# Optimization experiments

Hardware: AMD Instinct MI355X
Metric: run time of the kernel (lower is better)

Reference implementation:

```python
import jax, jax.numpy as jnp
import numpy as np

B, S, D = 8, 2048, 64
NEG = -1e9


def setup_inputs() -> dict:
    key = jax.random.key(0)
    kq, kk, kv = jax.random.split(key, 3)
    return {
        "queries": jax.random.normal(kq, (B, S, D), dtype=jnp.float32),
        "keys": jax.random.normal(kk, (B, S, D), dtype=jnp.float32),
        "values": jax.random.normal(kv, (B, S, D), dtype=jnp.float32),
        "mask_q": jnp.ones((B, S), dtype=jnp.float32),
        "mask_k": jnp.ones((B, S), dtype=jnp.float32),
        "mask_v": jnp.ones((B, S), dtype=jnp.float32),
    }


def reference(queries, keys, values, mask_q, mask_k, mask_v):
    # scaled QK^T: [B, Sq, Sk]
    scaler = jnp.sqrt(jnp.asarray(queries.shape[-1], dtype=queries.dtype))
    scores = jnp.einsum("bqd,bkd->bqk", queries, keys) / scaler
    # additive padding mask from outer product of query/key masks
    padding_mask = mask_q[:, :, None] * mask_k[:, None, :]  # [B, Sq, Sk]
    scores = scores + (1.0 - padding_mask) * NEG
    attention_weights = jax.nn.softmax(scores, axis=-1)
    # mask values then weighted sum
    values = values * mask_v[:, :, None]
    output = jnp.einsum("bqk,bkd->bqd", attention_weights, values)
    return output
```

## Files before the change

kernel.cpp:

```cpp
#include <hip/hip_runtime.h>
#include <math.h>

#define BATCH 8
#define SEQ   2048
#define DIM   64
#define NEGC  (-1e9f)

typedef short short8 __attribute__((ext_vector_type(8)));
typedef float f32x4  __attribute__((ext_vector_type(4)));

#define MFMA(a, b, c) __builtin_amdgcn_mfma_f32_16x16x32_bf16((a), (b), (c), 0, 0, 0)

__device__ __forceinline__ ushort f2bf(float x) {
    uint u = __float_as_uint(x);
    uint r = (u + 0x7fffu + ((u >> 16) & 1u)) >> 16;
    return (ushort)r;
}
__device__ __forceinline__ float bf2f(ushort h) {
    return __uint_as_float(((uint)h) << 16);
}

__global__ __launch_bounds__(256)
void prep_kv(const float* __restrict__ K, const float* __restrict__ V,
             const float* __restrict__ MV, ushort* __restrict__ ws) {
    const int gid = blockIdx.x * 256 + threadIdx.x;
    const int isV = gid >> 17;
    const int id  = gid & 131071;
    const int b   = id >> 14;
    const int rt  = id & 16383;
    const int t   = rt >> 9;
    const int r   = rt & 511;
    ushort* base = ws + (size_t)(b * 32 + t) * 12288;

    if (!isV) {
        const int mtc = r >> 6, qd = (r >> 4) & 3, mm = r & 15;
        const int mt = mtc >> 1, c = mtc & 1;
        const int key = t * 64 + mt * 16 + mm;
        const int d0  = c * 32 + qd * 8;
        const float* src = K + ((size_t)b * SEQ + key) * DIM + d0;
        float4 x0 = *(const float4*)src;
        float4 x1 = *(const float4*)(src + 4);
        float xs[8] = {x0.x, x0.y, x0.z, x0.w, x1.x, x1.y, x1.z, x1.w};
        short8 hv, lv;
#pragma unroll
        for (int j = 0; j < 8; j++) {
            ushort h = f2bf(xs[j]);
            hv[j] = (short)h;
            lv[j] = (short)f2bf(xs[j] - bf2f(h));
        }
        *(short8*)(base + r * 8)        = hv;
        *(short8*)(base + 4096 + r * 8) = lv;
    } else {
        const int kg5 = r >> 8, dg = (r >> 6) & 3, kq = (r >> 4) & 3, dm = r & 15;
        const int d  = dg * 16 + dm;
        const int k0 = t * 64 + kg5 * 32 + kq * 8;
        short8 ov;
#pragma unroll
        for (int j = 0; j < 8; j++) {
            const int key = k0 + j;
            float v = V[((size_t)b * SEQ + key) * DIM + d] * MV[(size_t)b * SEQ + key];
            ov[j] = (short)f2bf(v);
        }
        *(short8*)(base + 8192 + r * 8) = ov;
    }
}

__global__ __launch_bounds__(256, 2)
void attn_main(const float* __restrict__ Q, const float* __restrict__ MQ,
               const float* __restrict__ MK, const ushort* __restrict__ ws,
               float* __restrict__ O) {
    __shared__ __align__(16) ushort Stage[12288];
    __shared__ __align__(16) ushort Pf[4][512];
    __shared__ __align__(16) float  Msc[2][1280];

    const ushort* KfH = Stage;
    const ushort* KfL = Stage + 4096;
    const ushort* Vf  = Stage + 8192;

    const int t    = threadIdx.x;
    const int w    = t >> 6;
    const int lane = t & 63;
    const int quad = lane >> 4;
    const int lq   = lane & 15;
    const int qg   = w & 1;
    const int half = w >> 1;

    const int b  = blockIdx.x >> 6;
    const int q0 = (blockIdx.x & 63) * 32;
    const int q  = q0 + qg * 16 + lq;

    const float*  MKb = MK + (size_t)b * SEQ;
    const ushort* wsb = ws + (size_t)b * 32 * 12288;

    short8 qh[2], ql[2];
    {
        const float* Qr = Q + ((size_t)b * SEQ + q) * DIM;
#pragma unroll
        for (int c = 0; c < 2; c++) {
            float4 x0 = *(const float4*)(Qr + c * 32 + quad * 8);
            float4 x1 = *(const float4*)(Qr + c * 32 + quad * 8 + 4);
            float xs[8] = {x0.x, x0.y, x0.z, x0.w, x1.x, x1.y, x1.z, x1.w};
#pragma unroll
            for (int j = 0; j < 8; j++) {
                float v   = xs[j] * 0.125f;
                ushort hi = f2bf(v);
                ql[c][j]  = (short)f2bf(v - bf2f(hi));
                qh[c][j]  = (short)hi;
            }
        }
    }
    const float mq   = MQ[(size_t)b * SEQ + q];
    const float apen = NEGC * mq;

    float m = -1e30f, l = 0.0f;
    f32x4 ot0 = {0,0,0,0}, ot1 = {0,0,0,0}, ot2 = {0,0,0,0}, ot3 = {0,0,0,0};

    ushort* Pw   = Pf[w];
    const int kb = half * 32;

#pragma unroll 1
    for (int tile = 0; tile < 32; tile++) {
        const ushort* src = wsb + (size_t)tile * 12288;
#pragma unroll
        for (int u = 0; u < 6; u++) {
            const int off = (w * 64 + u * 256) * 8;
            __builtin_amdgcn_global_load_lds(
                (const __attribute__((address_space(1))) void*)(src + off + lane * 8),
                (__attribute__((address_space(3))) void*)(Stage + off),
                16, 0, 0);
        }
        __syncthreads();

        f32x4 st0 = {0,0,0,0}, st1 = {0,0,0,0};
        const int mtg = half * 2;
#pragma unroll
        for (int c = 0; c < 2; c++) {
            short8 a0h = *(const short8*)&KfH[((mtg + 0) * 2 + c) * 512 + lane * 8];
            short8 a0l = *(const short8*)&KfL[((mtg + 0) * 2 + c) * 512 + lane * 8];
            short8 a1h = *(const short8*)&KfH[((mtg + 1) * 2 + c) * 512 + lane * 8];
            short8 a1l = *(const short8*)&KfL[((mtg + 1) * 2 + c) * 512 + lane * 8];
            st0 = MFMA(a0h, qh[c], st0);
            st0 = MFMA(a0h, ql[c], st0);
            st0 = MFMA(a0l, qh[c], st0);
            st1 = MFMA(a1h, qh[c], st1);
            st1 = MFMA(a1h, ql[c], st1);
            st1 = MFMA(a1l, qh[c], st1);
        }

        const float* mkp = MKb + tile * 64 + kb + quad * 4;
        float4 mk0 = *(const float4*)mkp;
        float4 mk1 = *(const float4*)(mkp + 16);
        float mks0[4] = {mk0.x, mk0.y, mk0.z, mk0.w};
        float mks1[4] = {mk1.x, mk1.y, mk1.z, mk1.w};
        float s0[4], s1[4];
#pragma unroll
        for (int r = 0; r < 4; r++) {
            s0[r] = st0[r] + (NEGC - apen * mks0[r]);
            s1[r] = st1[r] + (NEGC - apen * mks1[r]);
        }
        float cm = s0[0];
#pragma unroll
        for (int r = 1; r < 4; r++) cm = fmaxf(cm, s0[r]);
#pragma unroll
        for (int r = 0; r < 4; r++) cm = fmaxf(cm, s1[r]);
        cm = fmaxf(cm, __shfl_xor(cm, 16));
        cm = fmaxf(cm, __shfl_xor(cm, 32));
        float nm    = fmaxf(m, cm);
        float alpha = __expf(m - nm);
        m = nm;

        float p0[4], p1[4], cs = 0.0f;
#pragma unroll
        for (int r = 0; r < 4; r++) { p0[r] = __expf(s0[r] - nm); cs += p0[r]; }
#pragma unroll
        for (int r = 0; r < 4; r++) { p1[r] = __expf(s1[r] - nm); cs += p1[r]; }
        cs += __shfl_xor(cs, 16);
        cs += __shfl_xor(cs, 32);
        l   = l * alpha + cs;
        ot0 *= alpha; ot1 *= alpha; ot2 *= alpha; ot3 *= alpha;

        uint2 pw0, pw1;
        pw0.x = (uint)f2bf(p0[0]) | ((uint)f2bf(p0[1]) << 16);
        pw0.y = (uint)f2bf(p0[2]) | ((uint)f2bf(p0[3]) << 16);
        pw1.x = (uint)f2bf(p1[0]) | ((uint)f2bf(p1[1]) << 16);
        pw1.y = (uint)f2bf(p1[2]) | ((uint)f2bf(p1[3]) << 16);
        int pidx0 = ((0 * 2 + (quad >> 1)) * 16 + lq) * 8 + (quad & 1) * 4;
        int pidx1 = ((1 * 2 + (quad >> 1)) * 16 + lq) * 8 + (quad & 1) * 4;
        *(uint2*)&Pw[pidx0] = pw0;
        *(uint2*)&Pw[pidx1] = pw1;
        short8 pfr = *(const short8*)&Pw[lane * 8];

        short8 v0 = *(const short8*)&Vf[(half * 4 + 0) * 512 + lane * 8];
        short8 v1 = *(const short8*)&Vf[(half * 4 + 1) * 512 + lane * 8];
        short8 v2 = *(const short8*)&Vf[(half * 4 + 2) * 512 + lane * 8];
        short8 v3 = *(const short8*)&Vf[(half * 4 + 3) * 512 + lane * 8];
        ot0 = MFMA(v0, pfr, ot0);
        ot1 = MFMA(v1, pfr, ot1);
        ot2 = MFMA(v2, pfr, ot2);
        ot3 = MFMA(v3, pfr, ot3);

        __syncthreads();
    }

    if (half == 1) {
        float* sc = &Msc[qg][lane * 20];
        *(f32x4*)&sc[0]  = ot0;
        *(f32x4*)&sc[4]  = ot1;
        *(f32x4*)&sc[8]  = ot2;
        *(f32x4*)&sc[12] = ot3;
        sc[16] = m;
        sc[17] = l;
    }
    __syncthreads();
    if (half == 0) {
        const float* sc = &Msc[qg][lane * 20];
        f32x4 ob0 = *(const f32x4*)&sc[0];
        f32x4 ob1 = *(const f32x4*)&sc[4];
        f32x4 ob2 = *(const f32x4*)&sc[8];
        f32x4 ob3 = *(const f32x4*)&sc[12];
        float mb = sc[16], lb = sc[17];

        float nm  = fmaxf(m, mb);
        float fa  = __expf(m - nm);
        float fb  = __expf(mb - nm);
        float inv = 1.0f / (l * fa + lb * fb);

        float* Orow = O + ((size_t)b * SEQ + q) * DIM;
        *(f32x4*)(Orow + 0  + quad * 4) = (ot0 * fa + ob0 * fb) * inv;
        *(f32x4*)(Orow + 16 + quad * 4) = (ot1 * fa + ob1 * fb) * inv;
        *(f32x4*)(Orow + 32 + quad * 4) = (ot2 * fa + ob2 * fb) * inv;
        *(f32x4*)(Orow + 48 + quad * 4) = (ot3 * fa + ob3 * fb) * inv;
    }
}

extern "C" void kernel_launch(void* const* d_in, const int* in_sizes, int n_in,
                              void* d_out, int out_size, void* d_ws, size_t ws_size,
                              hipStream_t stream) {
    const float* Q  = (const float*)d_in[0];
    const float* K  = (const float*)d_in[1];
    const float* V  = (const float*)d_in[2];
    const float* MQ = (const float*)d_in[3];
    const float* MK = (const float*)d_in[4];
    const float* MV = (const float*)d_in[5];
    float* O   = (float*)d_out;
    ushort* ws = (ushort*)d_ws;

    prep_kv<<<dim3(1024), dim3(256), 0, stream>>>(K, V, MV, ws);
    attn_main<<<dim3(BATCH * (SEQ / 32)), dim3(256), 0, stream>>>(Q, MQ, MK, ws, O);
}
```

Baseline: 119.1 us.

## Double-buffer KV tiles, drop K low-part, use 512-thread blocks and LDS-staged prep

The attention kernel now double-buffers the K/V tile in LDS, prefetching the next tile and its key mask while computing the current one, so only one barrier per tile remains. The K low-order bf16 split is dropped, cutting QK MFMAs from 3 to 2 per chunk and shrinking the workspace. Blocks grow to 512 threads covering 64 queries. The prep kernel transposes through shared memory for coalesced reads. Dropping the K residual term lowers score precision, which is a risk for the accuracy check. The epilogue region is partly hidden, so the Msc merge for the 8-wave layout cannot be fully verified.

```diff
diff --git a/kernel.cpp b/kernel.cpp
--- a/kernel.cpp
+++ b/kernel.cpp
@@ -1,4 +1,5 @@
 #include <hip/hip_runtime.h>
+#include <hip/hip_bf16.h>
 #include <math.h>
 
 #define BATCH 8
@@ -23,74 +24,80 @@
 __global__ __launch_bounds__(256)
 void prep_kv(const float* __restrict__ K, const float* __restrict__ V,
              const float* __restrict__ MV, ushort* __restrict__ ws) {
-    const int gid = blockIdx.x * 256 + threadIdx.x;
-    const int isV = gid >> 17;
-    const int id  = gid & 131071;
-    const int b   = id >> 14;
-    const int rt  = id & 16383;
-    const int t   = rt >> 9;
-    const int r   = rt & 511;
-    ushort* base = ws + (size_t)(b * 32 + t) * 12288;
-
-    if (!isV) {
-        const int mtc = r >> 6, qd = (r >> 4) & 3, mm = r & 15;
-        const int mt = mtc >> 1, c = mtc & 1;
-        const int key = t * 64 + mt * 16 + mm;
-        const int d0  = c * 32 + qd * 8;
-        const float* src = K + ((size_t)b * SEQ + key) * DIM + d0;
-        float4 x0 = *(const float4*)src;
-        float4 x1 = *(const float4*)(src + 4);
+    __shared__ float raw[64 * 68];
+    const int t    = threadIdx.x;
+    const int b    = blockIdx.x >> 5;
+    const int tile = blockIdx.x & 31;
+    const float* Kb  = K  + ((size_t)b * SEQ + tile * 64) * DIM;
+    const float* Vb  = V  + ((size_t)b * SEQ + tile * 64) * DIM;
+    const float* MVb = MV + (size_t)b * SEQ + tile * 64;
+    ushort* wsI = ws + (size_t)(b * 32 + tile) * 8192;
+
+#pragma unroll
+    for (int u = 0; u < 4; u++) {
+        int f = t + 256 * u, key = f >> 4, d4 = (f & 15) * 4;
+        *(float4*)&raw[key * 68 + d4] = *(const float4*)(Kb + (size_t)f * 4);
+    }
+    __syncthreads();
+#pragma unroll
+    for (int u = 0; u < 2; u++) {
+        int r = t + 256 * u;
+        int mtc = r >> 6, qd = (r >> 4) & 3, mm = r & 15;
+        int mt = mtc >> 1, c = mtc & 1;
+        int key = mt * 16 + mm, d0 = c * 32 + qd * 8;
+        float4 x0 = *(float4*)&raw[key * 68 + d0];
+        float4 x1 = *(float4*)&raw[key * 68 + d0 + 4];
         float xs[8] = {x0.x, x0.y, x0.z, x0.w, x1.x, x1.y, x1.z, x1.w};
-        short8 hv, lv;
-#pragma unroll
-        for (int j = 0; j < 8; j++) {
-            ushort h = f2bf(xs[j]);
-            hv[j] = (short)h;
-            lv[j] = (short)f2bf(xs[j] - bf2f(h));
-        }
-        *(short8*)(base + r * 8)        = hv;
-        *(short8*)(base + 4096 + r * 8) = lv;
-    } else {
-        const int kg5 = r >> 8, dg = (r >> 6) & 3, kq = (r >> 4) & 3, dm = r & 15;
-        const int d  = dg * 16 + dm;
-        const int k0 = t * 64 + kg5 * 32 + kq * 8;
+        short8 hv;
+#pragma unroll
+        for (int j = 0; j < 8; j++) hv[j] = (short)f2bf(xs[j]);
+        *(short8*)(wsI + r * 8) = hv;
+    }
+    __syncthreads();
+
+#pragma unroll
+    for (int u = 0; u < 4; u++) {
+        int f = t + 256 * u, key = f >> 4, d4 = (f & 15) * 4;
+        float4 x = *(const float4*)(Vb + (size_t)f * 4);
+        float mv = MVb[key];
+        x.x *= mv; x.y *= mv; x.z *= mv; x.w *= mv;
+        *(float4*)&raw[key * 68 + d4] = x;
+    }
+    __syncthreads();
+#pragma unroll
+    for (int u = 0; u < 2; u++) {
+        int r = t + 256 * u;
+        int kg5 = r >> 8, dg = (r >> 6) & 3, kq = (r >> 4) & 3, dm = r & 15;
+        int d = dg * 16 + dm, k0 = kg5 * 32 + kq * 8;
         short8 ov;
 #pragma unroll
-        for (int j = 0; j < 8; j++) {
-            const int key = k0 + j;
-            float v = V[((size_t)b * SEQ + key) * DIM + d] * MV[(size_t)b * SEQ + key];
-            ov[j] = (short)f2bf(v);
-        }
-        *(short8*)(base + 8192 + r * 8) = ov;
-    }
-}
-
-__global__ __launch_bounds__(256, 2)
+        for (int j = 0; j < 8; j++) ov[j] = (short)f2bf(raw[(k0 + j) * 68 + d]);
+        *(short8*)(wsI + 4096 + r * 8) = ov;
+    }
+}
+
+__global__ __launch_bounds__(512, 2)
 void attn_main(const float* __restrict__ Q, const float* __restrict__ MQ,
                const float* __restrict__ MK, const ushort* __restrict__ ws,
                float* __restrict__ O) {
-    __shared__ __align__(16) ushort Stage[12288];
-    __shared__ __align__(16) ushort Pf[4][512];
-    __shared__ __align__(16) float  Msc[2][1280];
-
-    const ushort* KfH = Stage;
-    const ushort* KfL = Stage + 4096;
-    const ushort* Vf  = Stage + 8192;
+    __shared__ __align__(16) ushort Stage[2][8192];
+    __shared__ __align__(16) ushort Pf[8][512];
+    __shared__ __align__(16) float  Msc[4][1280];
 
     const int t    = threadIdx.x;
     const int w    = t >> 6;
     const int lane = t & 63;
     const int quad = lane >> 4;
     const int lq   = lane & 15;
-    const int qg   = w & 1;
-    const int half = w >> 1;
-
-    const int b  = blockIdx.x >> 6;
-    const int q0 = (blockIdx.x & 63) * 32;
+    const int qg   = w & 3;
+    const int half = w >> 2;
+
+    const int b  = blockIdx.x >> 5;
+    const int q0 = (blockIdx.x & 31) * 64;
     const int q  = q0 + qg * 16 + lq;
 
     const float*  MKb = MK + (size_t)b * SEQ;
-    const ushort* wsb = ws + (size_t)b * 32 * 12288;
+    const ushort* wsb = ws + (size_t)b * 32 * 8192;
 
     short8 qh[2], ql[2];
     {
@@ -118,45 +125,59 @@
     ushort* Pw   = Pf[w];
     const int kb = half * 32;
 
+#pragma unroll
+    for (int u = 0; u < 2; u++) {
+        const int off = u * 4096 + w * 512;
+        __builtin_amdgcn_global_load_lds(
+            (const __attribute__((address_space(1))) void*)(wsb + off + lane * 8),
+            (__attribute__((address_space(3))) void*)(&Stage[0][0] + off),
+            16, 0, 0);
+    }
+    __syncthreads();
+
+    f32x4 mkA = *(const f32x4*)(MKb + kb + quad * 4);
+    f32x4 mkB = *(const f32x4*)(MKb + kb + 16 + quad * 4);
+
 #pragma unroll 1
     for (int tile = 0; tile < 32; tile++) {
-        const ushort* src = wsb + (size_t)tile * 12288;
-#pragma unroll
-        for (int u = 0; u < 6; u++) {
-            const int off = (w * 64 + u * 256) * 8;
-            __builtin_amdgcn_global_load_lds(
-                (const __attribute__((address_space(1))) void*)(src + off + lane * 8),
-                (__attribute__((address_space(3))) void*)(Stage + off),
-                16, 0, 0);
-        }
-        __syncthreads();
+        const ushort* cur = &Stage[tile & 1][0];
+
+        if (tile + 1 < 32) {
+            const ushort* src = wsb + (size_t)(tile + 1) * 8192;
+            ushort* dst = &Stage[(tile + 1) & 1][0];
+#pragma unroll
+            for (int u = 0; u < 2; u++) {
+                const int off = u * 4096 + w * 512;
+                __builtin_amdgcn_global_load_lds(
+                    (const __attribute__((address_space(1))) void*)(src + off + lane * 8),
+                    (__attribute__((address_space(3))) void*)(dst + off),
+                    16, 0, 0);
+            }
+        }
+        f32x4 nA = mkA, nB = mkB;
+        if (tile + 1 < 32) {
+            const float* mkp = MKb + (tile + 1) * 64 + kb + quad * 4;
+            nA = *(const f32x4*)mkp;
+            nB = *(const f32x4*)(mkp + 16);
+        }
 
         f32x4 st0 = {0,0,0,0}, st1 = {0,0,0,0};
         const int mtg = half * 2;
 #pragma unroll
         for (int c = 0; c < 2; c++) {
-            short8 a0h = *(const short8*)&KfH[((mtg + 0) * 2 + c) * 512 + lane * 8];
-            short8 a0l = *(const short8*)&KfL[((mtg + 0) * 2 + c) * 512 + lane * 8];
-            short8 a1h = *(const short8*)&KfH[((mtg + 1) * 2 + c) * 512 + lane * 8];
-            short8 a1l = *(const short8*)&KfL[((mtg + 1) * 2 + c) * 512 + lane * 8];
-            st0 = MFMA(a0h, qh[c], st0);
-            st0 = MFMA(a0h, ql[c], st0);
-            st0 = MFMA(a0l, qh[c], st0);
-            st1 = MFMA(a1h, qh[c], st1);
-            st1 = MFMA(a1h, ql[c], st1);
-            st1 = MFMA(a1l, qh[c], st1);
-        }
-
-        const float* mkp = MKb + tile * 64 + kb + quad * 4;
-        float4 mk0 = *(const float4*)mkp;
-        float4 mk1 = *(const float4*)(mkp + 16);
-        float mks0[4] = {mk0.x, mk0.y, mk0.z, mk0.w};
-        float mks1[4] = {mk1.x, mk1.y, mk1.z, mk1.w};
+            short8 a0 = *(const short8*)&cur[((mtg + 0) * 2 + c) * 512 + lane * 8];
+            short8 a1 = *(const short8*)&cur[((mtg + 1) * 2 + c) * 512 + lane * 8];
+            st0 = MFMA(a0, qh[c], st0);
+            st0 = MFMA(a0, ql[c], st0);
+            st1 = MFMA(a1, qh[c], st1);
+            st1 = MFMA(a1, ql[c], st1);
+        }
+
         float s0[4], s1[4];
 #pragma unroll
         for (int r = 0; r < 4; r++) {
-            s0[r] = st0[r] + (NEGC - apen * mks0[r]);
-            s1[r] = st1[r] + (NEGC - apen * mks1[r]);
+            s0[r] = st0[r] + (NEGC - apen * mkA[r]);
+            s1[r] = st1[r] + (NEGC - apen * mkB[r]);
         }
         float cm = s0[0];
 #pragma unroll
@@ -179,26 +200,32 @@
         l   = l * alpha + cs;
         ot0 *= alpha; ot1 *= alpha; ot2 *= alpha; ot3 *= alpha;
 
+        __hip_bfloat162 c0 = __float22bfloat162_rn(make_float2(p0[0], p0[1]));
+        __hip_bfloat162 c1 = __float22bfloat162_rn(make_float2(p0[2], p0[3]));
+        __hip_bfloat162 c2 = __float22bfloat162_rn(make_float2(p1[0], p1[1]));
+        __hip_bfloat162 c3 = __float22bfloat162_rn(make_float2(p1[2], p1[3]));
         uint2 pw0, pw1;
-        pw0.x = (uint)f2bf(p0[0]) | ((uint)f2bf(p0[1]) << 16);
-        pw0.y = (uint)f2bf(p0[2]) | ((uint)f2bf(p0[3]) << 16);
-        pw1.x = (uint)f2bf(p1[0]) | ((uint)f2bf(p1[1]) << 16);
-        pw1.y = (uint)f2bf(p1[2]) | ((uint)f2bf(p1[3]) << 16);
+        __builtin_memcpy(&pw0.x, &c0, 4);
+        __builtin_memcpy(&pw0.y, &c1, 4);
+        __builtin_memcpy(&pw1.x, &c2, 4);
+        __builtin_memcpy(&pw1.y, &c3, 4);
         int pidx0 = ((0 * 2 + (quad >> 1)) * 16 + lq) * 8 + (quad & 1) * 4;
         int pidx1 = ((1 * 2 + (quad >> 1)) * 16 + lq) * 8 + (quad & 1) * 4;
         *(uint2*)&Pw[pidx0] = pw0;
         *(uint2*)&Pw[pidx1] = pw1;
         short8 pfr = *(const short8*)&Pw[lane * 8];
 
-        short8 v0 = *(const short8*)&Vf[(half * 4 + 0) * 512 + lane * 8];
-        short8 v1 = *(const short8*)&Vf[(half * 4 + 1) * 512 + lane * 8];
-        short8 v2 = *(const short8*)&Vf[(half * 4 + 2) * 512 + lane * 8];
-        short8 v3 = *(const short8*)&Vf[(half * 4 + 3) * 512 + lane * 8];
+        const ushort* VfC = cur + 4096;
+        short8 v0 = *(const short8*)&VfC[(half * 4 + 0) * 512 + lane * 8];
+        short8 v1 = *(const short8*)&VfC[(half * 4 + 1) * 512 + lane * 8];
+        short8 v2 = *(const short8*)&VfC[(half * 4 + 2) * 512 + lane * 8];
+        short8 v3 = *(const short8*)&VfC[(half * 4 + 3) * 512 + lane * 8];
         ot0 = MFMA(v0, pfr, ot0);
         ot1 = MFMA(v1, pfr, ot1);
         ot2 = MFMA(v2, pfr, ot2);
         ot3 = MFMA(v3, pfr, ot3);
 
+        mkA = nA; mkB = nB;
         __syncthreads();
     }
 
@@ -245,6 +272,6 @@
     float* O   = (float*)d_out;
     ushort* ws = (ushort*)d_ws;
 
-    prep_kv<<<dim3(1024), dim3(256), 0, stream>>>(K, V, MV, ws);
-    attn_main<<<dim3(BATCH * (SEQ / 32)), dim3(256), 0, stream>>>(Q, MQ, MK, ws, O);
-}
+    prep_kv<<<dim3(256), dim3(256), 0, stream>>>(K, V, MV, ws);
+    attn_main<<<dim3(BATCH * (SEQ / 64)), dim3(512), 0, stream>>>(Q, MQ, MK, ws, O);
+}
```

Measured after the change: 108.5 us. 8.9% less time.
